# Performance work log

Hardware: AMD Instinct MI355X
Metric: run time of the kernel (lower is better)

The kernel has to match this reference:

```python
import jax, jax.numpy as jnp
import numpy as np

NUM_HEADS = 16


def setup_inputs() -> dict:
    key = jax.random.key(0)
    k0, k1, k2, k3 = jax.random.split(key, 4)
    S, dim = 8192, 1280              # packed vision tokens, embed dim
    H = NUM_HEADS
    D = dim // H                      # head_dim = 80
    n_seg = 8                         # 8 images x 1024 patches
    L = S // n_seg
    return {
        "hidden_states": jax.random.normal(k0, (S, dim), jnp.float32),
        "rotary_pos_emb": jax.random.normal(k1, (S, D // 2), jnp.float32),
        "w_qkv": jax.random.normal(k2, (3 * dim, dim), jnp.float32) * 0.02,
        "b_qkv": jnp.zeros((3 * dim,), jnp.float32),
        "w_proj": jax.random.normal(k3, (dim, dim), jnp.float32) * 0.02,
        "b_proj": jnp.zeros((dim,), jnp.float32),
        "cu_seqlens": jnp.arange(n_seg + 1, dtype=jnp.int32) * L,
    }


def _rotate_half(x):
    x1, x2 = jnp.split(x, 2, axis=-1)
    return jnp.concatenate([-x2, x1], axis=-1)


def _apply_rope(t, freqs):
    # t: [S, H, D]; freqs: [S, D//2]. Matches cat+rotate_half formulation
    # (cos/sin repeated to full head_dim), computed in float32.
    emb = jnp.concatenate([freqs, freqs], axis=-1)          # [S, D]
    cos = jnp.cos(emb)[:, None, :]                          # [S, 1, D]
    sin = jnp.sin(emb)[:, None, :]
    return t * cos + _rotate_half(t) * sin


def reference(hidden_states, rotary_pos_emb, w_qkv, b_qkv, w_proj, b_proj, cu_seqlens):
    S, dim = hidden_states.shape
    H = NUM_HEADS
    D = dim // H
    n_seg = cu_seqlens.shape[0] - 1   # equal-length packed segments
    L = S // n_seg

    qkv = hidden_states @ w_qkv.T + b_qkv                   # [S, 3*dim]
    q, k, v = jnp.split(qkv, 3, axis=-1)
    q = q.reshape(S, H, D)
    k = k.reshape(S, H, D)
    v = v.reshape(S, H, D)

    q = _apply_rope(q, rotary_pos_emb)
    k = _apply_rope(k, rotary_pos_emb)

    # block-diagonal varlen attention: batch over segments instead of an
    # [S, S] dense mask (honors the cu_seqlens sparsity structure)
    qs = q.reshape(n_seg, L, H, D)
    ks = k.reshape(n_seg, L, H, D)
    vs = v.reshape(n_seg, L, H, D)
    scale = D ** -0.5
    scores = jnp.einsum('blhd,bthd->bhlt', qs, ks) * scale  # [n_seg, H, L, L]
    probs = jax.nn.softmax(scores, axis=-1)
    ctx = jnp.einsum('bhlt,bthd->blhd', probs, vs)          # [n_seg, L, H, D]
    ctx = ctx.reshape(S, dim)

    return ctx @ w_proj.T + b_proj                          # [S, dim]
```

## Files before the change

### kernel.cpp

```cpp
#include <hip/hip_runtime.h>
#include <hip/hip_bf16.h>
#include <math.h>

#define S_TOK   8192
#define DIM     1280
#define NHEAD   16
#define HDIM    80
#define NSEG    8
#define SEGLEN  1024
#define QKV_LD  3840
#define DPAD    96

typedef __attribute__((ext_vector_type(8))) short bf16x8;
typedef __attribute__((ext_vector_type(4))) float f32x4;

__device__ __forceinline__ short f2b(float x) {
  __hip_bfloat16 h = __float2bfloat16(x);
  return *reinterpret_cast<short*>(&h);
}
__device__ __forceinline__ float b2f(short x) {
  __hip_bfloat16 h;
  *reinterpret_cast<short*>(&h) = x;
  return __bfloat162float(h);
}

__device__ __forceinline__ void gl_lds16(const void* g, void* l) {
  __builtin_amdgcn_global_load_lds(
      (const __attribute__((address_space(1))) unsigned int*)g,
      (__attribute__((address_space(3))) unsigned int*)l, 16, 0, 0);
}

__global__ __launch_bounds__(256) void cast_f32_bf16(
    const float* __restrict__ in, short* __restrict__ out, int n4)
{
  const int i = blockIdx.x * 256 + threadIdx.x;
  if (i >= n4) return;
  const float4 v = ((const float4*)in)[i];
  short4 o;
  o.x = f2b(v.x); o.y = f2b(v.y); o.z = f2b(v.z); o.w = f2b(v.w);
  ((short4*)out)[i] = o;
}

template<bool OUT_BF16>
__global__ __launch_bounds__(256) void gemm_mfma_nt(
    const short* __restrict__ A, const short* __restrict__ B,
    const float* __restrict__ bias, void* __restrict__ Cout,
    int M, int N, int K)
{
  __shared__ short As[128 * 32];
  __shared__ short Bs[128 * 32];
  const int t = threadIdx.x;
  const int wave = t >> 6, lane = t & 63;
  const int q = lane >> 4, r = lane & 15;
  const int bm = blockIdx.y * 128, bn = blockIdx.x * 128;
  const int wr = (wave >> 1) * 64, wc = (wave & 1) * 64;

  f32x4 acc[4][4];
#pragma unroll
  for (int i = 0; i < 4; ++i)
#pragma unroll
    for (int j = 0; j < 4; ++j) acc[i][j] = (f32x4)(0.f);

  for (int k0 = 0; k0 < K; k0 += 32) {
    __syncthreads();
#pragma unroll
    for (int i = 0; i < 2; ++i) {
      const int c = i * 256 + t;
      const int row = c >> 2, off = (c & 3) * 8;
      gl_lds16(A + (size_t)(bm + row) * K + k0 + off, As + c * 8);
      gl_lds16(B + (size_t)(bn + row) * K + k0 + off, Bs + c * 8);
    }
    __syncthreads();

    bf16x8 af[4], bg[4];
#pragma unroll
    for (int mt = 0; mt < 4; ++mt)
      af[mt] = *(const bf16x8*)&As[(wr + mt * 16 + r) * 32 + q * 8];
#pragma unroll
    for (int nt = 0; nt < 4; ++nt)
      bg[nt] = *(const bf16x8*)&Bs[(wc + nt * 16 + r) * 32 + q * 8];
#pragma unroll
    for (int mt = 0; mt < 4; ++mt)
#pragma unroll
      for (int nt = 0; nt < 4; ++nt)
        acc[mt][nt] = __builtin_amdgcn_mfma_f32_16x16x32_bf16(
            af[mt], bg[nt], acc[mt][nt], 0, 0, 0);
  }

#pragma unroll
  for (int mt = 0; mt < 4; ++mt)
#pragma unroll
    for (int nt = 0; nt < 4; ++nt)
#pragma unroll
      for (int reg = 0; reg < 4; ++reg) {
        const int mrow = bm + wr + mt * 16 + q * 4 + reg;
        const int ncol = bn + wc + nt * 16 + r;
        const float v = acc[mt][nt][reg] + bias[ncol];
        if (OUT_BF16)
          ((short*)Cout)[(size_t)mrow * N + ncol] = f2b(v);
        else
          ((float*)Cout)[(size_t)mrow * N + ncol] = v;
      }
}

__global__ __launch_bounds__(256) void rope_cast(
    const short* __restrict__ qkvb, const float* __restrict__ rot,
    short* __restrict__ Qb, short* __restrict__ Kb)
{
  const int idx = blockIdx.x * 256 + threadIdx.x;
  const int j = idx % 48;
  const int h = (idx / 48) % NHEAD;
  const int s = idx / (48 * NHEAD);
  short* qo = Qb + ((size_t)s * NHEAD + h) * DPAD;
  short* ko = Kb + ((size_t)s * NHEAD + h) * DPAD;
  if (j < 40) {
    const float f = rot[s * 40 + j];
    const float c = cosf(f), sn = sinf(f);
    const short* qi = qkvb + (size_t)s * QKV_LD + h * HDIM;
    const short* ki = qi + DIM;
    const float scale = 0.11180339887498949f;
    const float q0 = b2f(qi[j]), q1 = b2f(qi[j + 40]);
    qo[j]      = f2b((q0 * c - q1 * sn) * scale);
    qo[j + 40] = f2b((q1 * c + q0 * sn) * scale);
    const float k0 = b2f(ki[j]), k1 = b2f(ki[j + 40]);
    ko[j]      = f2b(k0 * c - k1 * sn);
    ko[j + 40] = f2b(k1 * c + k0 * sn);
  } else {
    const int z = 80 + (j - 40);
    qo[z] = 0; qo[z + 8] = 0;
    ko[z] = 0; ko[z + 8] = 0;
  }
}

__global__ __launch_bounds__(256) void v_transpose(
    const short* __restrict__ qkvb, short* __restrict__ Vt)
{
  const int tid = blockIdx.x * 256 + threadIdx.x;
  const int c   = tid >> 13;
  const int kv  = tid & 8191;
  const int head = c / 10;
  const int d0   = (c % 10) * 8;
  const int seg  = kv >> 10;
  const bf16x8 v = *(const bf16x8*)(qkvb + (size_t)kv * QKV_LD + 2 * DIM +
                                    head * HDIM + d0);
  short* ob = Vt + ((size_t)(seg * NHEAD + head) * HDIM + d0) * SEGLEN + (kv & 1023);
#pragma unroll
  for (int j = 0; j < 8; ++j)
    ob[(size_t)j * SEGLEN] = v[j];
}

#define LQK 104
#define LVT 72
#define LPR 72
#define NT  16

__global__ __launch_bounds__(256, 3) void attn_mfma(
    const short* __restrict__ Qb, const short* __restrict__ Kb,
    const short* __restrict__ Vtg, short* __restrict__ ctxb)
{
  __shared__ short Ks[64 * LQK];
  __shared__ short Vs[80 * LVT];
  __shared__ short Ps[4][32 * LPR];

  const int t = threadIdx.x;
  const int wave = t >> 6, lane = t & 63;
  const int q = lane >> 4, r = lane & 15;
  const int seg = blockIdx.z, head = blockIdx.y;
  const int m0 = blockIdx.x * 128;
  const size_t srow0 = (size_t)seg * SEGLEN;
  const size_t vbase = (size_t)(seg * NHEAD + head) * HDIM * SEGLEN;

  bf16x8 qf[2][3];
#pragma unroll
  for (int mt = 0; mt < 2; ++mt)
#pragma unroll
    for (int ks = 0; ks < 3; ++ks)
      qf[mt][ks] = *(const bf16x8*)(
          Qb + ((srow0 + m0 + wave * 32 + mt * 16 + r) * NHEAD + head) * DPAD +
          ks * 32 + q * 8);

  float m_[2][4], l_[2][4];
  f32x4 o[2][5];
#pragma unroll
  for (int mt = 0; mt < 2; ++mt) {
#pragma unroll
    for (int i = 0; i < 4; ++i) { m_[mt][i] = -1e30f; l_[mt][i] = 0.f; }
#pragma unroll
    for (int i = 0; i < 5; ++i) o[mt][i] = (f32x4)(0.f);
  }

  bf16x8 kreg[3], vreg[3];
  const int kc_row[3] = {(0 * 256 + t) / 12, (1 * 256 + t) / 12, (2 * 256 + t) / 12};
  const int kc_off[3] = {((0 * 256 + t) % 12) * 8, ((1 * 256 + t) % 12) * 8,
                         ((2 * 256 + t) % 12) * 8};

#define LOAD_TILE(n0)                                                          \
  {                                                                            \
    _Pragma("unroll")                                                          \
    for (int i = 0; i < 3; ++i)                                                \
      kreg[i] = *(const bf16x8*)(                                              \
          Kb + ((srow0 + (n0) + kc_row[i]) * NHEAD + head) * DPAD + kc_off[i]);\
    _Pragma("unroll")                                                          \
    for (int i = 0; i < 3; ++i) {                                              \
      const int c = i * 256 + t;                                               \
      if (c < 640)                                                             \
        vreg[i] = *(const bf16x8*)(Vtg + vbase + (size_t)(c >> 3) * SEGLEN +   \
                                   (n0) + (c & 7) * 8);                        \
    }                                                                          \
  }

  LOAD_TILE(0)

  for (int tile = 0; tile < NT; ++tile) {
    __syncthreads();
#pragma unroll
    for (int i = 0; i < 3; ++i)
      *(bf16x8*)&Ks[kc_row[i] * LQK + kc_off[i]] = kreg[i];
#pragma unroll
    for (int i = 0; i < 3; ++i) {
      const int c = i * 256 + t;
      if (c < 640)
        *(bf16x8*)&Vs[(c >> 3) * LVT + (c & 7) * 8] = vreg[i];
    }
    __syncthreads();

    if (tile + 1 < NT) LOAD_TILE((tile + 1) * 64)

    f32x4 s[2][4];
#pragma unroll
    for (int mt = 0; mt < 2; ++mt)
#pragma unroll
      for (int nt = 0; nt < 4; ++nt) s[mt][nt] = (f32x4)(0.f);
    __builtin_amdgcn_s_setprio(1);
#pragma unroll
    for (int ks = 0; ks < 3; ++ks)
#pragma unroll
      for (int nt = 0; nt < 4; ++nt) {
        const bf16x8 kf = *(const bf16x8*)&Ks[(nt * 16 + r) * LQK + ks * 32 + q * 8];
        s[0][nt] = __builtin_amdgcn_mfma_f32_16x16x32_bf16(qf[0][ks], kf, s[0][nt], 0, 0, 0);
        s[1][nt] = __builtin_amdgcn_mfma_f32_16x16x32_bf16(qf[1][ks], kf, s[1][nt], 0, 0, 0);
      }
    __builtin_amdgcn_s_setprio(0);

#pragma unroll
    for (int mt = 0; mt < 2; ++mt)
#pragma unroll
      for (int reg = 0; reg < 4; ++reg) {
        float sm = fmaxf(fmaxf(s[mt][0][reg], s[mt][1][reg]),
                         fmaxf(s[mt][2][reg], s[mt][3][reg]));
#pragma unroll
        for (int off = 1; off < 16; off <<= 1)
          sm = fmaxf(sm, __shfl_xor(sm, off));
        const float mn = fmaxf(m_[mt][reg], sm);
        const float corr = __expf(m_[mt][reg] - mn);
        m_[mt][reg] = mn;
        float ps = 0.f;
#pragma unroll
        for (int nt = 0; nt < 4; ++nt) {
          const float e = __expf(s[mt][nt][reg] - mn);
          s[mt][nt][reg] = e;
          ps += e;
        }
#pragma unroll
        for (int off = 1; off < 16; off <<= 1)
          ps += __shfl_xor(ps, off);
        l_[mt][reg] = l_[mt][reg] * corr + ps;
#pragma unroll
        for (int dt = 0; dt < 5; ++dt) o[mt][dt][reg] *= corr;
      }

#pragma unroll
    for (int mt = 0; mt < 2; ++mt)
#pragma unroll
      for (int nt = 0; nt < 4; ++nt)
#pragma unroll
        for (int reg = 0; reg < 4; ++reg)
          Ps[wave][(mt * 16 + q * 4 + reg) * LPR + nt * 16 + r] =
              f2b(s[mt][nt][reg]);

    __builtin_amdgcn_s_setprio(1);
#pragma unroll
    for (int ks2 = 0; ks2 < 2; ++ks2) {
      const bf16x8 pf0 = *(const bf16x8*)&Ps[wave][r * LPR + ks2 * 32 + q * 8];
      const bf16x8 pf1 = *(const bf16x8*)&Ps[wave][(16 + r) * LPR + ks2 * 32 + q * 8];
#pragma unroll
      for (int dt = 0; dt < 5; ++dt) {
        const bf16x8 vf = *(const bf16x8*)&Vs[(dt * 16 + r) * LVT + ks2 * 32 + q * 8];
        o[0][dt] = __builtin_amdgcn_mfma_f32_16x16x32_bf16(pf0, vf, o[0][dt], 0, 0, 0);
        o[1][dt] = __builtin_amdgcn_mfma_f32_16x16x32_bf16(pf1, vf, o[1][dt], 0, 0, 0);
      }
    }
    __builtin_amdgcn_s_setprio(0);
  }

#pragma unroll
  for (int mt = 0; mt < 2; ++mt)
#pragma unroll
    for (int reg = 0; reg < 4; ++reg) {
      const float inv = 1.f / l_[mt][reg];
      const size_t row = srow0 + m0 + wave * 32 + mt * 16 + q * 4 + reg;
#pragma unroll
      for (int dt = 0; dt < 5; ++dt)
        ctxb[row * DIM + head * HDIM + dt * 16 + r] = f2b(o[mt][dt][reg] * inv);
    }
}

extern "C" void kernel_launch(void* const* d_in, const int* in_sizes, int n_in,
                              void* d_out, int out_size, void* d_ws, size_t ws_size,
                              hipStream_t stream)
{
  const float* hs    = (const float*)d_in[0];
  const float* rot   = (const float*)d_in[1];
  const float* wqkv  = (const float*)d_in[2];
  const float* bqkv  = (const float*)d_in[3];
  const float* wproj = (const float*)d_in[4];
  const float* bproj = (const float*)d_in[5];
  float* out = (float*)d_out;

  char* w = (char*)d_ws;
  short* hs_b    = (short*)w;  w += (size_t)S_TOK * DIM * 2;
  short* wqkv_b  = (short*)w;  w += (size_t)QKV_LD * DIM * 2;
  short* wproj_b = (short*)w;  w += (size_t)DIM * DIM * 2;
  short* qkv_b   = (short*)w;  w += (size_t)S_TOK * QKV_LD * 2;
  short* Qb      = (short*)w;  w += (size_t)S_TOK * NHEAD * DPAD * 2;
  short* Kb      = (short*)w;  w += (size_t)S_TOK * NHEAD * DPAD * 2;
  short* ctx_b   = (short*)w;  w += (size_t)S_TOK * DIM * 2;
  short* Vt_g    = hs_b;

  dim3 blk(256);

  cast_f32_bf16<<<dim3(S_TOK * DIM / 4 / 256), blk, 0, stream>>>(hs, hs_b, S_TOK * DIM / 4);
  cast_f32_bf16<<<dim3(QKV_LD * DIM / 4 / 256), blk, 0, stream>>>(wqkv, wqkv_b, QKV_LD * DIM / 4);
  cast_f32_bf16<<<dim3(DIM * DIM / 4 / 256), blk, 0, stream>>>(wproj, wproj_b, DIM * DIM / 4);

  gemm_mfma_nt<true><<<dim3(QKV_LD / 128, S_TOK / 128), blk, 0, stream>>>(
      hs_b, wqkv_b, bqkv, qkv_b, S_TOK, QKV_LD, DIM);

  rope_cast<<<dim3(S_TOK * NHEAD * 48 / 256), blk, 0, stream>>>(qkv_b, rot, Qb, Kb);

  v_transpose<<<dim3(160 * S_TOK / 256), blk, 0, stream>>>(qkv_b, Vt_g);

  attn_mfma<<<dim3(SEGLEN / 128, NHEAD, NSEG), blk, 0, stream>>>(Qb, Kb, Vt_g, ctx_b);

  gemm_mfma_nt<false><<<dim3(DIM / 128, S_TOK / 128), blk, 0, stream>>>(
      ctx_b, wproj_b, bproj, out, S_TOK, DIM, DIM);
}
```

Before: 523.9 us.

## Rewrite attention with 32x32 MFMA transposed scores and register-resident P

The attention kernel moves from 16x16x32 to 32x32x16 bf16 MFMA, computing S^T so each lane owns a query column. That lets P be repacked into B-operand fragments with cross-half shuffles instead of a per-wave LDS round trip. Softmax switches to exp2 with log2(e) folded into the Q scale, and the output rescale is skipped when no row max grows. Each block now covers 256 queries with fewer blocks and a 2-wave-occupancy bound. The cost is more registers, a zero-padded V tile up to 96 wide, and less grid parallelism (512 blocks).

```diff
diff --git a/kernel.cpp b/kernel.cpp
--- a/kernel.cpp
+++ b/kernel.cpp
@@ -11,8 +11,9 @@
 #define QKV_LD  3840
 #define DPAD    96
 
-typedef __attribute__((ext_vector_type(8))) short bf16x8;
-typedef __attribute__((ext_vector_type(4))) float f32x4;
+typedef __attribute__((ext_vector_type(8)))  short bf16x8;
+typedef __attribute__((ext_vector_type(4)))  float f32x4;
+typedef __attribute__((ext_vector_type(16))) float f32x16;
 
 __device__ __forceinline__ short f2b(float x) {
   __hip_bfloat16 h = __float2bfloat16(x);
@@ -118,7 +119,7 @@
     const float c = cosf(f), sn = sinf(f);
     const short* qi = qkvb + (size_t)s * QKV_LD + h * HDIM;
     const short* ki = qi + DIM;
-    const float scale = 0.11180339887498949f;
+    const float scale = 0.11180339887498949f * 1.4426950408889634f;
     const float q0 = b2f(qi[j]), q1 = b2f(qi[j + 40]);
     qo[j]      = f2b((q0 * c - q1 * sn) * scale);
     qo[j + 40] = f2b((q1 * c + q0 * sn) * scale);
@@ -151,158 +152,207 @@
 
 #define LQK 104
 #define LVT 72
-#define LPR 72
-#define NT  16
-
-__global__ __launch_bounds__(256, 3) void attn_mfma(
+#define NTILE 16
+
+__global__ __launch_bounds__(256, 2) void attn_mfma(
     const short* __restrict__ Qb, const short* __restrict__ Kb,
     const short* __restrict__ Vtg, short* __restrict__ ctxb)
 {
   __shared__ short Ks[64 * LQK];
-  __shared__ short Vs[80 * LVT];
-  __shared__ short Ps[4][32 * LPR];
+  __shared__ short Vs[96 * LVT];
 
   const int t = threadIdx.x;
   const int wave = t >> 6, lane = t & 63;
-  const int q = lane >> 4, r = lane & 15;
+  const int c = lane & 31, hi = lane >> 5;
   const int seg = blockIdx.z, head = blockIdx.y;
-  const int m0 = blockIdx.x * 128;
+  const int m0 = blockIdx.x * 256;
   const size_t srow0 = (size_t)seg * SEGLEN;
   const size_t vbase = (size_t)(seg * NHEAD + head) * HDIM * SEGLEN;
 
-  bf16x8 qf[2][3];
-#pragma unroll
-  for (int mt = 0; mt < 2; ++mt)
-#pragma unroll
-    for (int ks = 0; ks < 3; ++ks)
-      qf[mt][ks] = *(const bf16x8*)(
-          Qb + ((srow0 + m0 + wave * 32 + mt * 16 + r) * NHEAD + head) * DPAD +
-          ks * 32 + q * 8);
-
-  float m_[2][4], l_[2][4];
-  f32x4 o[2][5];
-#pragma unroll
-  for (int mt = 0; mt < 2; ++mt) {
-#pragma unroll
-    for (int i = 0; i < 4; ++i) { m_[mt][i] = -1e30f; l_[mt][i] = 0.f; }
-#pragma unroll
-    for (int i = 0; i < 5; ++i) o[mt][i] = (f32x4)(0.f);
-  }
-
-  bf16x8 kreg[3], vreg[3];
+  for (int i = t; i < 16 * LVT / 2; i += 256)
+    ((int*)(Vs + 80 * LVT))[i] = 0;
+
+  bf16x8 qf[2][6];
+#pragma unroll
+  for (int u = 0; u < 2; ++u)
+#pragma unroll
+    for (int ks = 0; ks < 6; ++ks)
+      qf[u][ks] = *(const bf16x8*)(
+          Qb + ((srow0 + m0 + wave * 64 + u * 32 + c) * NHEAD + head) * DPAD +
+          ks * 16 + hi * 8);
+
+  f32x16 o[3][2];
+#pragma unroll
+  for (int d = 0; d < 3; ++d)
+#pragma unroll
+    for (int u = 0; u < 2; ++u) o[d][u] = (f32x16)(0.f);
+  float m_[2] = {-1e30f, -1e30f}, l_[2] = {0.f, 0.f};
+
   const int kc_row[3] = {(0 * 256 + t) / 12, (1 * 256 + t) / 12, (2 * 256 + t) / 12};
   const int kc_off[3] = {((0 * 256 + t) % 12) * 8, ((1 * 256 + t) % 12) * 8,
                          ((2 * 256 + t) % 12) * 8};
-
-#define LOAD_TILE(n0)                                                          \
+  bf16x8 kreg[3], vreg[3];
+
+#define LOAD_K(n0)                                                             \
   {                                                                            \
     _Pragma("unroll")                                                          \
     for (int i = 0; i < 3; ++i)                                                \
       kreg[i] = *(const bf16x8*)(                                              \
           Kb + ((srow0 + (n0) + kc_row[i]) * NHEAD + head) * DPAD + kc_off[i]);\
+  }
+#define LOAD_V(n0)                                                             \
+  {                                                                            \
     _Pragma("unroll")                                                          \
     for (int i = 0; i < 3; ++i) {                                              \
-      const int c = i * 256 + t;                                               \
-      if (c < 640)                                                             \
-        vreg[i] = *(const bf16x8*)(Vtg + vbase + (size_t)(c >> 3) * SEGLEN +   \
-                                   (n0) + (c & 7) * 8);                        \
+      const int cc = i * 256 + t;                                              \
+      if (cc < 640)                                                            \
+        vreg[i] = *(const bf16x8*)(Vtg + vbase + (size_t)(cc >> 3) * SEGLEN +  \
+                                   (n0) + (cc & 7) * 8);                       \
     }                                                                          \
   }
 
-  LOAD_TILE(0)
-
-  for (int tile = 0; tile < NT; ++tile) {
+  LOAD_K(0)
+  LOAD_V(0)
+
+  for (int tile = 0; tile < NTILE; ++tile) {
     __syncthreads();
 #pragma unroll
     for (int i = 0; i < 3; ++i)
       *(bf16x8*)&Ks[kc_row[i] * LQK + kc_off[i]] = kreg[i];
 #pragma unroll
     for (int i = 0; i < 3; ++i) {
-      const int c = i * 256 + t;
-      if (c < 640)
-        *(bf16x8*)&Vs[(c >> 3) * LVT + (c & 7) * 8] = vreg[i];
+      const int cc = i * 256 + t;
+      if (cc < 640)
+        *(bf16x8*)&Vs[(cc >> 3) * LVT + (cc & 7) * 8] = vreg[i];
     }
     __syncthreads();
 
-    if (tile + 1 < NT) LOAD_TILE((tile + 1) * 64)
-
-    f32x4 s[2][4];
-#pragma unroll
-    for (int mt = 0; mt < 2; ++mt)
-#pragma unroll
-      for (int nt = 0; nt < 4; ++nt) s[mt][nt] = (f32x4)(0.f);
+    if (tile + 1 < NTILE) LOAD_K((tile + 1) * 64)
+
+    f32x16 s[2][2];
+#pragma unroll
+    for (int tt = 0; tt < 2; ++tt)
+#pragma unroll
+      for (int u = 0; u < 2; ++u) s[tt][u] = (f32x16)(0.f);
     __builtin_amdgcn_s_setprio(1);
 #pragma unroll
-    for (int ks = 0; ks < 3; ++ks)
-#pragma unroll
-      for (int nt = 0; nt < 4; ++nt) {
-        const bf16x8 kf = *(const bf16x8*)&Ks[(nt * 16 + r) * LQK + ks * 32 + q * 8];
-        s[0][nt] = __builtin_amdgcn_mfma_f32_16x16x32_bf16(qf[0][ks], kf, s[0][nt], 0, 0, 0);
-        s[1][nt] = __builtin_amdgcn_mfma_f32_16x16x32_bf16(qf[1][ks], kf, s[1][nt], 0, 0, 0);
+    for (int tt = 0; tt < 2; ++tt)
+#pragma unroll
+      for (int ks = 0; ks < 6; ++ks) {
+        const bf16x8 kf =
+            *(const bf16x8*)&Ks[(tt * 32 + c) * LQK + ks * 16 + hi * 8];
+        s[tt][0] = __builtin_amdgcn_mfma_f32_32x32x16_bf16(kf, qf[0][ks], s[tt][0], 0, 0, 0);
+        s[tt][1] = __builtin_amdgcn_mfma_f32_32x32x16_bf16(kf, qf[1][ks], s[tt][1], 0, 0, 0);
       }
     __builtin_amdgcn_s_setprio(0);
 
-#pragma unroll
-    for (int mt = 0; mt < 2; ++mt)
-#pragma unroll
-      for (int reg = 0; reg < 4; ++reg) {
-        float sm = fmaxf(fmaxf(s[mt][0][reg], s[mt][1][reg]),
-                         fmaxf(s[mt][2][reg], s[mt][3][reg]));
-#pragma unroll
-        for (int off = 1; off < 16; off <<= 1)
-          sm = fmaxf(sm, __shfl_xor(sm, off));
-        const float mn = fmaxf(m_[mt][reg], sm);
-        const float corr = __expf(m_[mt][reg] - mn);
-        m_[mt][reg] = mn;
-        float ps = 0.f;
-#pragma unroll
-        for (int nt = 0; nt < 4; ++nt) {
-          const float e = __expf(s[mt][nt][reg] - mn);
-          s[mt][nt][reg] = e;
-          ps += e;
+    bf16x8 pf[2][4];
+#pragma unroll
+    for (int u = 0; u < 2; ++u) {
+      float a0 = -1e30f, a1 = -1e30f, a2 = -1e30f, a3 = -1e30f;
+#pragma unroll
+      for (int tt = 0; tt < 2; ++tt)
+#pragma unroll
+        for (int i = 0; i < 16; i += 4) {
+          a0 = fmaxf(a0, s[tt][u][i]);
+          a1 = fmaxf(a1, s[tt][u][i + 1]);
+          a2 = fmaxf(a2, s[tt][u][i + 2]);
+          a3 = fmaxf(a3, s[tt][u][i + 3]);
         }
-#pragma unroll
-        for (int off = 1; off < 16; off <<= 1)
-          ps += __shfl_xor(ps, off);
-        l_[mt][reg] = l_[mt][reg] * corr + ps;
-#pragma unroll
-        for (int dt = 0; dt < 5; ++dt) o[mt][dt][reg] *= corr;
-      }
-
-#pragma unroll
-    for (int mt = 0; mt < 2; ++mt)
-#pragma unroll
-      for (int nt = 0; nt < 4; ++nt)
-#pragma unroll
-        for (int reg = 0; reg < 4; ++reg)
-          Ps[wave][(mt * 16 + q * 4 + reg) * LPR + nt * 16 + r] =
-              f2b(s[mt][nt][reg]);
+      float mx = fmaxf(fmaxf(a0, a1), fmaxf(a2, a3));
+      mx = fmaxf(mx, __shfl_xor(mx, 32));
+      if (!__all(mx <= m_[u])) {
+        const float mn = fmaxf(m_[u], mx);
+        const float corr = exp2f(m_[u] - mn);
+        m_[u] = mn;
+        l_[u] *= corr;
+#pragma unroll
+        for (int d = 0; d < 3; ++d)
+#pragma unroll
+          for (int i = 0; i < 16; ++i) o[d][u][i] *= corr;
+      }
+      float s0 = 0.f, s1 = 0.f, s2 = 0.f, s3 = 0.f;
+#pragma unroll
+      for (int tt = 0; tt < 2; ++tt)
+#pragma unroll
+        for (int i = 0; i < 16; i += 4) {
+          const float e0 = exp2f(s[tt][u][i] - m_[u]);
+          const float e1 = exp2f(s[tt][u][i + 1] - m_[u]);
+          const float e2 = exp2f(s[tt][u][i + 2] - m_[u]);
+          const float e3 = exp2f(s[tt][u][i + 3] - m_[u]);
+          s[tt][u][i] = e0; s[tt][u][i + 1] = e1;
+          s[tt][u][i + 2] = e2; s[tt][u][i + 3] = e3;
+          s0 += e0; s1 += e1; s2 += e2; s3 += e3;
+        }
+      float sum = (s0 + s1) + (s2 + s3);
+      sum += __shfl_xor(sum, 32);
+      l_[u] += sum;
+
+      unsigned d8[2][8];
+#pragma unroll
+      for (int tt = 0; tt < 2; ++tt)
+#pragma unroll
+        for (int i = 0; i < 8; ++i)
+          d8[tt][i] = ((unsigned)(unsigned short)f2b(s[tt][u][2 * i + 1]) << 16) |
+                      (unsigned short)f2b(s[tt][u][2 * i]);
+      unsigned rcv[2][8 / 2];
+#pragma unroll
+      for (int tt = 0; tt < 2; ++tt) {
+        const unsigned sd0 = hi ? d8[tt][0] : d8[tt][2];
+        const unsigned sd1 = hi ? d8[tt][1] : d8[tt][3];
+        const unsigned sd2 = hi ? d8[tt][4] : d8[tt][6];
+        const unsigned sd3 = hi ? d8[tt][5] : d8[tt][7];
+        rcv[tt][0] = __shfl_xor((int)sd0, 32);
+        rcv[tt][1] = __shfl_xor((int)sd1, 32);
+        rcv[tt][2] = __shfl_xor((int)sd2, 32);
+        rcv[tt][3] = __shfl_xor((int)sd3, 32);
+      }
+#pragma unroll
+      for (int ks = 0; ks < 4; ++ks) {
+        const int tt = ks >> 1, k2 = ks & 1;
+        int4 pw;
+        pw.x = hi ? (int)rcv[tt][2 * k2]     : (int)d8[tt][4 * k2];
+        pw.y = hi ? (int)rcv[tt][2 * k2 + 1] : (int)d8[tt][4 * k2 + 1];
+        pw.z = hi ? (int)d8[tt][4 * k2 + 2]  : (int)rcv[tt][2 * k2];
+        pw.w = hi ? (int)d8[tt][4 * k2 + 3]  : (int)rcv[tt][2 * k2 + 1];
+        pf[u][ks] = *reinterpret_cast<bf16x8*>(&pw);
+      }
+    }
+
+    if (tile + 1 < NTILE) LOAD_V((tile + 1) * 64)
 
     __builtin_amdgcn_s_setprio(1);
 #pragma unroll
-    for (int ks2 = 0; ks2 < 2; ++ks2) {
-      const bf16x8 pf0 = *(const bf16x8*)&Ps[wave][r * LPR + ks2 * 32 + q * 8];
-      const bf16x8 pf1 = *(const bf16x8*)&Ps[wave][(16 + r) * LPR + ks2 * 32 + q * 8];
-#pragma unroll
-      for (int dt = 0; dt < 5; ++dt) {
-        const bf16x8 vf = *(const bf16x8*)&Vs[(dt * 16 + r) * LVT + ks2 * 32 + q * 8];
-        o[0][dt] = __builtin_amdgcn_mfma_f32_16x16x32_bf16(pf0, vf, o[0][dt], 0, 0, 0);
-        o[1][dt] = __builtin_amdgcn_mfma_f32_16x16x32_bf16(pf1, vf, o[1][dt], 0, 0, 0);
-      }
-    }
+    for (int dt = 0; dt < 3; ++dt)
+#pragma unroll
+      for (int ks = 0; ks < 4; ++ks) {
+        const bf16x8 vf =
+            *(const bf16x8*)&Vs[(dt * 32 + c) * LVT + ks * 16 + hi * 8];
+        o[dt][0] = __builtin_amdgcn_mfma_f32_32x32x16_bf16(vf, pf[0][ks], o[dt][0], 0, 0, 0);
+        o[dt][1] = __builtin_amdgcn_mfma_f32_32x32x16_bf16(vf, pf[1][ks], o[dt][1], 0, 0, 0);
+      }
     __builtin_amdgcn_s_setprio(0);
   }
 
 #pragma unroll
-  for (int mt = 0; mt < 2; ++mt)
-#pragma unroll
-    for (int reg = 0; reg < 4; ++reg) {
-      const float inv = 1.f / l_[mt][reg];
-      const size_t row = srow0 + m0 + wave * 32 + mt * 16 + q * 4 + reg;
-#pragma unroll
-      for (int dt = 0; dt < 5; ++dt)
-        ctxb[row * DIM + head * HDIM + dt * 16 + r] = f2b(o[mt][dt][reg] * inv);
-    }
+  for (int u = 0; u < 2; ++u) {
+    const float inv = 1.f / l_[u];
+    const size_t row = srow0 + m0 + wave * 64 + u * 32 + c;
+#pragma unroll
+    for (int dt = 0; dt < 3; ++dt)
+#pragma unroll
+      for (int g = 0; g < 4; ++g) {
+        const int d0 = dt * 32 + 8 * g + 4 * hi;
+        if (d0 < HDIM) {
+          short4 v4;
+          v4.x = f2b(o[dt][u][4 * g + 0] * inv);
+          v4.y = f2b(o[dt][u][4 * g + 1] * inv);
+          v4.z = f2b(o[dt][u][4 * g + 2] * inv);
+          v4.w = f2b(o[dt][u][4 * g + 3] * inv);
+          *(short4*)&ctxb[row * DIM + head * HDIM + d0] = v4;
+        }
+      }
+  }
 }
 
 extern "C" void kernel_launch(void* const* d_in, const int* in_sizes, int n_in,
@@ -340,7 +390,7 @@
 
   v_transpose<<<dim3(160 * S_TOK / 256), blk, 0, stream>>>(qkv_b, Vt_g);
 
-  attn_mfma<<<dim3(SEGLEN / 128, NHEAD, NSEG), blk, 0, stream>>>(Qb, Kb, Vt_g, ctx_b);
+  attn_mfma<<<dim3(SEGLEN / 256, NHEAD, NSEG), blk, 0, stream>>>(Qb, Kb, Vt_g, ctx_b);
 
   gemm_mfma_nt<false><<<dim3(DIM / 128, S_TOK / 128), blk, 0, stream>>>(
       ctx_b, wproj_b, bproj, out, S_TOK, DIM, DIM);
```

New measurement: 459.0 us. 1.14x faster.
